# Kernel optimization log

Measured on AMD Instinct MI355X. Metric: run time of the kernel, lower is better.

## Reference

```python
import jax, jax.numpy as jnp
import numpy as np

D_MODEL = 1024
NUM_HEADS = 16
DEPTH = D_MODEL // NUM_HEADS
MAX_SEQ = 2048
B, S = 2, 2048


def setup_inputs() -> dict:
    key = jax.random.key(0)
    ks = jax.random.split(key, 12)
    scale = 1.0 / np.sqrt(D_MODEL)
    inp = {
        'q': jax.random.normal(ks[0], (B, S, D_MODEL), jnp.float32),
        'k': jax.random.normal(ks[1], (B, S, D_MODEL), jnp.float32),
        'v': jax.random.normal(ks[2], (B, S, D_MODEL), jnp.float32),
        'mask': jnp.zeros((B, 1, S, S), jnp.float32),
        'wq_w': jax.random.normal(ks[3], (D_MODEL, D_MODEL), jnp.float32) * scale,
        'wq_b': jnp.zeros((D_MODEL,), jnp.float32),
        'wk_w': jax.random.normal(ks[4], (D_MODEL, D_MODEL), jnp.float32) * scale,
        'wk_b': jnp.zeros((D_MODEL,), jnp.float32),
        'wv_w': jax.random.normal(ks[5], (D_MODEL, D_MODEL), jnp.float32) * scale,
        'wv_b': jnp.zeros((D_MODEL,), jnp.float32),
        'dense_w': jax.random.normal(ks[6], (D_MODEL, D_MODEL), jnp.float32) * scale,
        'dense_b': jnp.zeros((D_MODEL,), jnp.float32),
        'rel_bias': jax.random.normal(ks[7], (2 * MAX_SEQ - 1, NUM_HEADS), jnp.float32),
    }
    return inp


def _split_heads(x):
    # [B, S, D_MODEL] -> [B, H, S, depth]
    b, s, _ = x.shape
    return x.reshape(b, s, NUM_HEADS, DEPTH).transpose(0, 2, 1, 3)


def reference(q, k, v, mask, wq_w, wq_b, wk_w, wk_b, wv_w, wv_b, dense_w, dense_b, rel_bias):
    b, s, _ = q.shape
    # torch Linear: y = x @ W.T + b
    qh = _split_heads(q @ wq_w.T + wq_b)
    kh = _split_heads(k @ wk_w.T + wk_b)
    vh = _split_heads(v @ wv_w.T + wv_b)
    logits = jnp.einsum('bhqd,bhkd->bhqk', qh, kh) / jnp.sqrt(jnp.float32(DEPTH))
    # relative position bias gather
    pos = jnp.arange(s)
    idx = jnp.clip(pos[:, None] - pos[None, :] + MAX_SEQ - 1, 0, 2 * MAX_SEQ - 2)  # [S, S]
    pos_bias = rel_bias[idx]                      # [S, S, H]
    pos_bias = pos_bias.transpose(2, 0, 1)[None]  # [1, H, S, S]
    logits = logits + pos_bias + mask * (-1e9)
    attn = jax.nn.softmax(logits, axis=-1)        # dropout is identity in eval
    out = jnp.einsum('bhqk,bhkd->bhqd', attn, vh)
    out = out.transpose(0, 2, 1, 3).reshape(b, s, D_MODEL)
    out = out @ dense_w.T + dense_b
    return out, attn
```

## Files before the change

kernel.cpp:

```cpp
#include <hip/hip_runtime.h>

typedef _Float16 f16x8 __attribute__((ext_vector_type(8)));
typedef _Float16 f16x4 __attribute__((ext_vector_type(4)));
typedef float f32x4 __attribute__((ext_vector_type(4)));
typedef unsigned short u16x8 __attribute__((ext_vector_type(8)));
typedef unsigned int u32;

#define MFMA16H(a, b, c) __builtin_amdgcn_mfma_f32_16x16x32_f16(a, b, c, 0, 0, 0)

#if __has_builtin(__builtin_amdgcn_exp2f)
#define EXP2F(x) __builtin_amdgcn_exp2f(x)
#else
#define EXP2F(x) exp2f(x)
#endif

#define LOG2E 1.44269504088896340736f
#define SHIFT2 14.0f

__device__ __forceinline__ unsigned short f2bf(float x) {
  unsigned u = __float_as_uint(x);
  u += 0x7FFF + ((u >> 16) & 1);
  return (unsigned short)(u >> 16);
}
__device__ __forceinline__ float bf2f(unsigned short h) {
  return __uint_as_float(((unsigned)h) << 16);
}
__device__ __forceinline__ f16x8 ldh8(const _Float16* p) {
  return *reinterpret_cast<const f16x8*>(p);
}
__device__ __forceinline__ u16x8 ldu8(const unsigned short* p) {
  return *reinterpret_cast<const u16x8*>(p);
}
__device__ __forceinline__ f16x8 cvt8(float4 a, float4 b) {
  f16x8 r;
  r[0] = (_Float16)a.x; r[1] = (_Float16)a.y; r[2] = (_Float16)a.z; r[3] = (_Float16)a.w;
  r[4] = (_Float16)b.x; r[5] = (_Float16)b.y; r[6] = (_Float16)b.z; r[7] = (_Float16)b.w;
  return r;
}

__global__ __launch_bounds__(256) void prep_mask_perm(const float* __restrict__ src,
                                                      unsigned short* __restrict__ dst) {
  const int blk = blockIdx.x;
  const int kt = blk & 31, bq = blk >> 5;
  const int b = bq >> 5, qt = bq & 31;
  const int lane = threadIdx.x;
  const int w = lane >> 6, lg = (lane >> 4) & 3, lr = lane & 15;
  const int q0 = qt * 64;
  const float cs = -1e9f * LOG2E;
  unsigned short vals[16];
#pragma unroll
  for (int c = 0; c < 4; ++c)
#pragma unroll
    for (int r = 0; r < 4; ++r) {
      const int qr = q0 + w * 16 + lg * 4 + r;
      const int kc = kt * 64 + c * 16 + lr;
      vals[c * 4 + r] = f2bf(src[((size_t)b * 2048 + qr) * 2048 + kc] * cs);
    }
  uint4* out = reinterpret_cast<uint4*>(dst) + ((size_t)blk * 256 + lane) * 2;
  out[0] = *reinterpret_cast<uint4*>(&vals[0]);
  out[1] = *reinterpret_cast<uint4*>(&vals[8]);
}

__global__ __launch_bounds__(256, 3) void proj_gemm_kernel(
    const float* __restrict__ qin, const float* __restrict__ kin, const float* __restrict__ vin,
    const float* __restrict__ wq, const float* __restrict__ wk, const float* __restrict__ wv,
    const float* __restrict__ bq, const float* __restrict__ bk, const float* __restrict__ bv,
    _Float16* __restrict__ qhf, _Float16* __restrict__ khf, _Float16* __restrict__ vhT) {
  __shared__ __align__(16) _Float16 As[128 * 32];
  __shared__ __align__(16) _Float16 Bs[128 * 32];

  const int mode = blockIdx.x >> 8;
  const int t = blockIdx.x & 255;
  const float* A = mode == 0 ? qin : (mode == 1 ? kin : vin);
  const float* B = mode == 0 ? wq : (mode == 1 ? wk : wv);
  const float* bias = mode == 0 ? bq : (mode == 1 ? bk : bv);
  _Float16* outp = mode == 0 ? qhf : (mode == 1 ? khf : vhT);

  const int tid = threadIdx.x;
  const int tm = t & 31, tn = t >> 5;
  const int m0 = tm * 128, n0 = tn * 128;
  const int w = tid >> 6, l = tid & 63, lg = l >> 4, lr = l & 15;
  const int wr = w >> 1, wc = w & 1;
  const int srow = tid >> 2, scol = (tid & 3) * 8;

  f32x4 acc[4][4] = {};

  for (int kt = 0; kt < 32; ++kt) {
    const int k0 = kt * 32;
    float4 ra[2][2], rb[2][2];
#pragma unroll
    for (int it = 0; it < 2; ++it) {
      const int row = it * 64 + srow;
      const float* pa = A + (size_t)(m0 + row) * 1024 + k0 + scol;
      const float* pb = B + (size_t)(n0 + row) * 1024 + k0 + scol;
      ra[it][0] = *reinterpret_cast<const float4*>(pa);
      ra[it][1] = *reinterpret_cast<const float4*>(pa + 4);
      rb[it][0] = *reinterpret_cast<const float4*>(pb);
      rb[it][1] = *reinterpret_cast<const float4*>(pb + 4);
    }
    __syncthreads();
#pragma unroll
    for (int it = 0; it < 2; ++it) {
      const int eo = (it * 256 + tid) * 8;
      *reinterpret_cast<f16x8*>(As + eo) = cvt8(ra[it][0], ra[it][1]);
      *reinterpret_cast<f16x8*>(Bs + eo) = cvt8(rb[it][0], rb[it][1]);
    }
    __syncthreads();

    f16x8 fa[4], fb[4];
#pragma unroll
    for (int i = 0; i < 4; ++i) {
      fa[i] = ldh8(As + (wr * 64 + i * 16 + lr) * 32 + lg * 8);
      fb[i] = ldh8(Bs + (wc * 64 + i * 16 + lr) * 32 + lg * 8);
    }
#pragma unroll
    for (int i = 0; i < 4; ++i)
#pragma unroll
      for (int j = 0; j < 4; ++j)
        acc[i][j] = MFMA16H(fa[i], fb[j], acc[i][j]);
  }

#pragma unroll
  for (int i = 0; i < 4; ++i) {
    const int mrow = m0 + wr * 64 + i * 16 + lg * 4;
#pragma unroll
    for (int j = 0; j < 4; ++j) {
      const int ncol = n0 + wc * 64 + j * 16 + lr;
      const float bv = bias[ncol];
#pragma unroll
      for (int r = 0; r < 4; ++r) {
        const int m = mrow + r;
        const float v = acc[i][j][r] + bv;
        const int bb = m >> 11, s = m & 2047, hh = ncol >> 6, d = ncol & 63;
        if (mode != 2)
          outp[((size_t)(bb * 16 + hh) * 2048 + s) * 64 + d] = (_Float16)v;
        else
          outp[((size_t)(bb * 16 + hh) * 64 + d) * 2048 + s] = (_Float16)v;
      }
    }
  }
}

__global__ __launch_bounds__(256) void dense_gemm_kernel(
    const _Float16* __restrict__ A, const float* __restrict__ B,
    const float* __restrict__ bias, float* __restrict__ out_f) {
  __shared__ __align__(16) _Float16 As[128 * 32];
  __shared__ __align__(16) _Float16 Bs[128 * 32];

  const int tid = threadIdx.x;
  const int tm = blockIdx.x & 31, tn = blockIdx.x >> 5;
  const int m0 = tm * 128, n0 = tn * 128;
  const int w = tid >> 6, l = tid & 63, lg = l >> 4, lr = l & 15;
  const int wr = w >> 1, wc = w & 1;
  const int srow = tid >> 2, scol = (tid & 3) * 8;

  f32x4 acc[4][4] = {};

  for (int kt = 0; kt < 32; ++kt) {
    const int k0 = kt * 32;
    uint4 ra[2];
    float4 rb[2][2];
#pragma unroll
    for (int it = 0; it < 2; ++it) {
      const int row = it * 64 + srow;
      ra[it] = *reinterpret_cast<const uint4*>(A + (size_t)(m0 + row) * 1024 + k0 + scol);
      const float* pb = B + (size_t)(n0 + row) * 1024 + k0 + scol;
      rb[it][0] = *reinterpret_cast<const float4*>(pb);
      rb[it][1] = *reinterpret_cast<const float4*>(pb + 4);
    }
    __syncthreads();
#pragma unroll
    for (int it = 0; it < 2; ++it) {
      const int eo = (it * 256 + tid) * 8;
      *reinterpret_cast<uint4*>(As + eo) = ra[it];
      *reinterpret_cast<f16x8*>(Bs + eo) = cvt8(rb[it][0], rb[it][1]);
    }
    __syncthreads();

    f16x8 fa[4], fb[4];
#pragma unroll
    for (int i = 0; i < 4; ++i) {
      fa[i] = ldh8(As + (wr * 64 + i * 16 + lr) * 32 + lg * 8);
      fb[i] = ldh8(Bs + (wc * 64 + i * 16 + lr) * 32 + lg * 8);
    }
#pragma unroll
    for (int i = 0; i < 4; ++i)
#pragma unroll
      for (int j = 0; j < 4; ++j)
        acc[i][j] = MFMA16H(fa[i], fb[j], acc[i][j]);
  }

#pragma unroll
  for (int i = 0; i < 4; ++i) {
    const int mrow = m0 + wr * 64 + i * 16 + lg * 4;
#pragma unroll
    for (int j = 0; j < 4; ++j) {
      const int ncol = n0 + wc * 64 + j * 16 + lr;
      const float bv = bias[ncol];
#pragma unroll
      for (int r = 0; r < 4; ++r)
        out_f[(size_t)(mrow + r) * 1024 + ncol] = acc[i][j][r] + bv;
    }
  }
}

__global__ __launch_bounds__(256, 3) void attn_pv_kernel(
    const _Float16* __restrict__ qh, const _Float16* __restrict__ kh,
    const _Float16* __restrict__ vT,
    const float* __restrict__ rel_bias, const unsigned short* __restrict__ mperm,
    _Float16* __restrict__ o_h, float* __restrict__ scal) {
  __shared__ float rb2[2112];
  __shared__ __align__(16) _Float16 p_lds[64 * 76];

  const int bid = blockIdx.x;
  const int wg = ((bid & 7) << 7) | (bid >> 3);
  const int bh = wg >> 5, qt = wg & 31;
  const int b = bh >> 4, h = bh & 15;
  const int q0 = qt * 64;
  const int tid = threadIdx.x;
  const int w = tid >> 6, l = tid & 63, lg = l >> 4, lr = l & 15;

  for (int t = tid; t < 2111; t += 256)
    rb2[t] = rel_bias[(q0 + t) * 16 + h] * LOG2E - SHIFT2;

  const size_t bh_off = (size_t)bh * 2048 * 64;
  const _Float16* qhb = qh + bh_off;
  const _Float16* khb = kh + bh_off;
  const _Float16* vTb = vT + bh_off;
  const unsigned short* mpb =
      mperm + (((size_t)(b * 32 + qt) * 32) * 256 + tid) * 16;

  f16x8 qf[2];
  {
    const size_t qrow = (size_t)(q0 + w * 16 + lr) * 64;
    qf[0] = ldh8(qhb + qrow + lg * 8);
    qf[1] = ldh8(qhb + qrow + 32 + lg * 8);
  }
  __syncthreads();

  const int qbase = w * 16 + lg * 4;
  const float c1 = 0.125f * LOG2E;
  float sacc[4] = {0.f, 0.f, 0.f, 0.f};
  f32x4 acc_o[4] = {};

  for (int kt = 0; kt < 32; ++kt) {
    u16x8 m0v = ldu8(mpb + (size_t)kt * 4096);
    u16x8 m1v = ldu8(mpb + (size_t)kt * 4096 + 8);
#pragma unroll
    for (int c = 0; c < 4; ++c) {
      const int kc = kt * 64 + c * 16 + lr;
      const _Float16* kr = khb + (size_t)kc * 64 + lg * 8;
      f32x4 acc = {};
      acc = MFMA16H(qf[0], ldh8(kr), acc);
      acc = MFMA16H(qf[1], ldh8(kr + 32), acc);
#pragma unroll
      for (int r = 0; r < 4; ++r) {
        const float mbf = bf2f((c < 2) ? (unsigned short)m0v[(c & 1) * 4 + r]
                                       : (unsigned short)m1v[(c & 1) * 4 + r]);
        const float l2 = fmaf(acc[r], c1, rb2[qbase + r - kc + 2047]) + mbf;
        const float p = EXP2F(l2);
        sacc[r] += p;
        p_lds[(qbase + r) * 76 + c * 16 + lr] = (_Float16)p;
      }
    }
    f16x8 pf0 = ldh8(p_lds + (w * 16 + lr) * 76 + lg * 8);
    f16x8 pf1 = ldh8(p_lds + (w * 16 + lr) * 76 + 32 + lg * 8);
#pragma unroll
    for (int n = 0; n < 4; ++n) {
      const _Float16* vr = vTb + (size_t)(n * 16 + lr) * 2048 + kt * 64 + lg * 8;
      acc_o[n] = MFMA16H(pf0, ldh8(vr), acc_o[n]);
      acc_o[n] = MFMA16H(pf1, ldh8(vr + 32), acc_o[n]);
    }
  }

  float inv_s[4];
#pragma unroll
  for (int r = 0; r < 4; ++r) {
    float s = sacc[r];
    s += __shfl_xor(s, 1);
    s += __shfl_xor(s, 2);
    s += __shfl_xor(s, 4);
    s += __shfl_xor(s, 8);
    inv_s[r] = 1.0f / s;
    if (lr == 0) scal[(size_t)bh * 2048 + q0 + qbase + r] = inv_s[r];
  }

#pragma unroll
  for (int n = 0; n < 4; ++n)
#pragma unroll
    for (int r = 0; r < 4; ++r) {
      const int qr = q0 + qbase + r;
      const int d = n * 16 + lr;
      o_h[((size_t)(b * 2048 + qr) * 16 + h) * 64 + d] = (_Float16)(acc_o[n][r] * inv_s[r]);
    }
}

__global__ __launch_bounds__(256, 4) void attn_write_kernel(
    const _Float16* __restrict__ qh, const _Float16* __restrict__ kh,
    const float* __restrict__ rel_bias, const unsigned short* __restrict__ mperm,
    const float* __restrict__ scal, float* __restrict__ attn_out) {
  __shared__ float rb2[2112];
  __shared__ __align__(16) float p32[64 * 68];

  const int bid = blockIdx.x;
  const int wg = ((bid & 7) << 7) | (bid >> 3);
  const int bh = wg >> 5, qt = wg & 31;
  const int b = bh >> 4, h = bh & 15;
  const int q0 = qt * 64;
  const int tid = threadIdx.x;
  const int w = tid >> 6, l = tid & 63, lg = l >> 4, lr = l & 15;

  for (int t = tid; t < 2111; t += 256)
    rb2[t] = rel_bias[(q0 + t) * 16 + h] * LOG2E - SHIFT2;

  const size_t bh_off = (size_t)bh * 2048 * 64;
  const _Float16* qhb = qh + bh_off;
  const _Float16* khb = kh + bh_off;
  const unsigned short* mpb =
      mperm + (((size_t)(b * 32 + qt) * 32) * 256 + tid) * 16;
  float* attn_bh = attn_out + (size_t)bh * 2048 * 2048;

  f16x8 qf[2];
  {
    const size_t qrow = (size_t)(q0 + w * 16 + lr) * 64;
    qf[0] = ldh8(qhb + qrow + lg * 8);
    qf[1] = ldh8(qhb + qrow + 32 + lg * 8);
  }
  __syncthreads();

  const int qbase = w * 16 + lg * 4;
  const float c1 = 0.125f * LOG2E;
  float4 inv4 = *reinterpret_cast<const float4*>(scal + (size_t)bh * 2048 + q0 + qbase);
  const float invs[4] = {inv4.x, inv4.y, inv4.z, inv4.w};

  const int srow = w * 16 + (l >> 2);
  const int scb = (l & 3) * 16;

  for (int kt = 0; kt < 32; ++kt) {
    u16x8 m0v = ldu8(mpb + (size_t)kt * 4096);
    u16x8 m1v = ldu8(mpb + (size_t)kt * 4096 + 8);
#pragma unroll
    for (int c = 0; c < 4; ++c) {
      const int kc = kt * 64 + c * 16 + lr;
      const _Float16* kr = khb + (size_t)kc * 64 + lg * 8;
      f32x4 acc = {};
      acc = MFMA16H(qf[0], ldh8(kr), acc);
      acc = MFMA16H(qf[1], ldh8(kr + 32), acc);
#pragma unroll
      for (int r = 0; r < 4; ++r) {
        const float mbf = bf2f((c < 2) ? (unsigned short)m0v[(c & 1) * 4 + r]
                                       : (unsigned short)m1v[(c & 1) * 4 + r]);
        const float l2 = fmaf(acc[r], c1, rb2[qbase + r - kc + 2047]) + mbf;
        p32[(qbase + r) * 68 + c * 16 + lr] = EXP2F(l2) * invs[r];
      }
    }
    float* arow = attn_bh + (size_t)(q0 + srow) * 2048 + kt * 64 + scb;
#pragma unroll
    for (int i = 0; i < 4; ++i)
      *reinterpret_cast<float4*>(arow + i * 4) =
          *reinterpret_cast<const float4*>(&p32[srow * 68 + scb + i * 4]);
  }
}

extern "C" void kernel_launch(void* const* d_in, const int* in_sizes, int n_in,
                              void* d_out, int out_size, void* d_ws, size_t ws_size,
                              hipStream_t stream) {
  const float* q = (const float*)d_in[0];
  const float* k = (const float*)d_in[1];
  const float* v = (const float*)d_in[2];
  const float* mask = (const float*)d_in[3];
  const float* wq_w = (const float*)d_in[4];
  const float* wq_b = (const float*)d_in[5];
  const float* wk_w = (const float*)d_in[6];
  const float* wk_b = (const float*)d_in[7];
  const float* wv_w = (const float*)d_in[8];
  const float* wv_b = (const float*)d_in[9];
  const float* dw = (const float*)d_in[10];
  const float* db = (const float*)d_in[11];
  const float* rel = (const float*)d_in[12];

  char* ws = (char*)d_ws;
  _Float16* qhf  = (_Float16*)(ws + 0);
  _Float16* khf  = (_Float16*)(ws + 8388608);
  _Float16* vhT  = (_Float16*)(ws + 16777216);
  _Float16* o_h  = (_Float16*)(ws + 25165824);
  float* scal    = (float*)(ws + 33554432);
  unsigned short* mperm = (unsigned short*)(ws + 33816576);

  float* out = (float*)d_out;
  float* attn_out = out + 4194304;

  prep_mask_perm<<<2048, 256, 0, stream>>>(mask, mperm);

  proj_gemm_kernel<<<768, 256, 0, stream>>>(q, k, v, wq_w, wk_w, wv_w,
                                            wq_b, wk_b, wv_b, qhf, khf, vhT);

  attn_pv_kernel<<<1024, 256, 0, stream>>>(qhf, khf, vhT, rel, mperm, o_h, scal);
  attn_write_kernel<<<1024, 256, 0, stream>>>(qhf, khf, rel, mperm, scal, attn_out);

  dense_gemm_kernel<<<256, 256, 0, stream>>>(o_h, dw, db, out);
}
```

Before: 606.7 us.

## Store unnormalized fp16 probabilities in PV pass and rescale in a streaming fixup kernel

The second attention kernel, which recomputed QK^T, bias and exp to write the fp32 attention matrix, is removed. The PV kernel now also writes unnormalized fp16 probabilities to a workspace buffer, and a grid-stride fixup kernel scales them by the stored inverse row sums into fp32. K and mask loads in the PV loop are double-buffered in registers, and occupancy is lowered to 2 blocks per CU to make room for them. The exp shift is reduced from 14 to 5 so fp16 probabilities keep enough range. This costs an extra 128MB fp16 write plus read, and the attention output now carries fp16 rounding.

```diff
diff --git a/kernel.cpp b/kernel.cpp
--- a/kernel.cpp
+++ b/kernel.cpp
@@ -15,7 +15,7 @@
 #endif
 
 #define LOG2E 1.44269504088896340736f
-#define SHIFT2 14.0f
+#define SHIFT2 5.0f
 
 __device__ __forceinline__ unsigned short f2bf(float x) {
   unsigned u = __float_as_uint(x);
@@ -204,11 +204,12 @@
   }
 }
 
-__global__ __launch_bounds__(256, 3) void attn_pv_kernel(
+__global__ __launch_bounds__(256, 2) void attn_pv_kernel(
     const _Float16* __restrict__ qh, const _Float16* __restrict__ kh,
     const _Float16* __restrict__ vT,
     const float* __restrict__ rel_bias, const unsigned short* __restrict__ mperm,
-    _Float16* __restrict__ o_h, float* __restrict__ scal) {
+    _Float16* __restrict__ o_h, _Float16* __restrict__ p16,
+    float* __restrict__ scal) {
   __shared__ float rb2[2112];
   __shared__ __align__(16) _Float16 p_lds[64 * 76];
 
@@ -229,6 +230,7 @@
   const _Float16* vTb = vT + bh_off;
   const unsigned short* mpb =
       mperm + (((size_t)(b * 32 + qt) * 32) * 256 + tid) * 16;
+  _Float16* pbh = p16 + (size_t)bh * 2048 * 2048;
 
   f16x8 qf[2];
   {
@@ -243,20 +245,30 @@
   float sacc[4] = {0.f, 0.f, 0.f, 0.f};
   f32x4 acc_o[4] = {};
 
-  for (int kt = 0; kt < 32; ++kt) {
-    u16x8 m0v = ldu8(mpb + (size_t)kt * 4096);
-    u16x8 m1v = ldu8(mpb + (size_t)kt * 4096 + 8);
+  f16x8 kA[8], kB[8];
+  u16x8 mA[2], mB[2];
+
+  auto loadK = [&](int kt, f16x8* kd, u16x8* md) {
+    md[0] = ldu8(mpb + (size_t)kt * 4096);
+    md[1] = ldu8(mpb + (size_t)kt * 4096 + 8);
 #pragma unroll
     for (int c = 0; c < 4; ++c) {
+      const _Float16* kr = khb + (size_t)(kt * 64 + c * 16 + lr) * 64 + lg * 8;
+      kd[c * 2] = ldh8(kr);
+      kd[c * 2 + 1] = ldh8(kr + 32);
+    }
+  };
+
+  auto step = [&](int kt, const f16x8* kd, const u16x8* md) {
+#pragma unroll
+    for (int c = 0; c < 4; ++c) {
+      f32x4 acc = {};
+      acc = MFMA16H(qf[0], kd[c * 2], acc);
+      acc = MFMA16H(qf[1], kd[c * 2 + 1], acc);
       const int kc = kt * 64 + c * 16 + lr;
-      const _Float16* kr = khb + (size_t)kc * 64 + lg * 8;
-      f32x4 acc = {};
-      acc = MFMA16H(qf[0], ldh8(kr), acc);
-      acc = MFMA16H(qf[1], ldh8(kr + 32), acc);
 #pragma unroll
       for (int r = 0; r < 4; ++r) {
-        const float mbf = bf2f((c < 2) ? (unsigned short)m0v[(c & 1) * 4 + r]
-                                       : (unsigned short)m1v[(c & 1) * 4 + r]);
+        const float mbf = bf2f((unsigned short)md[c >> 1][(c & 1) * 4 + r]);
         const float l2 = fmaf(acc[r], c1, rb2[qbase + r - kc + 2047]) + mbf;
         const float p = EXP2F(l2);
         sacc[r] += p;
@@ -265,12 +277,23 @@
     }
     f16x8 pf0 = ldh8(p_lds + (w * 16 + lr) * 76 + lg * 8);
     f16x8 pf1 = ldh8(p_lds + (w * 16 + lr) * 76 + 32 + lg * 8);
+    _Float16* prow = pbh + (size_t)(q0 + w * 16 + lr) * 2048 + kt * 64 + lg * 8;
+    *reinterpret_cast<f16x8*>(prow) = pf0;
+    *reinterpret_cast<f16x8*>(prow + 32) = pf1;
 #pragma unroll
     for (int n = 0; n < 4; ++n) {
       const _Float16* vr = vTb + (size_t)(n * 16 + lr) * 2048 + kt * 64 + lg * 8;
       acc_o[n] = MFMA16H(pf0, ldh8(vr), acc_o[n]);
       acc_o[n] = MFMA16H(pf1, ldh8(vr + 32), acc_o[n]);
     }
+  };
+
+  loadK(0, kA, mA);
+  for (int kt = 0; kt < 32; kt += 2) {
+    loadK(kt + 1, kB, mB);
+    step(kt, kA, mA);
+    loadK((kt + 2) & 31, kA, mA);
+    step(kt + 1, kB, mB);
   }
 
   float inv_s[4];
@@ -295,70 +318,20 @@
     }
 }
 
-__global__ __launch_bounds__(256, 4) void attn_write_kernel(
-    const _Float16* __restrict__ qh, const _Float16* __restrict__ kh,
-    const float* __restrict__ rel_bias, const unsigned short* __restrict__ mperm,
-    const float* __restrict__ scal, float* __restrict__ attn_out) {
-  __shared__ float rb2[2112];
-  __shared__ __align__(16) float p32[64 * 68];
-
-  const int bid = blockIdx.x;
-  const int wg = ((bid & 7) << 7) | (bid >> 3);
-  const int bh = wg >> 5, qt = wg & 31;
-  const int b = bh >> 4, h = bh & 15;
-  const int q0 = qt * 64;
-  const int tid = threadIdx.x;
-  const int w = tid >> 6, l = tid & 63, lg = l >> 4, lr = l & 15;
-
-  for (int t = tid; t < 2111; t += 256)
-    rb2[t] = rel_bias[(q0 + t) * 16 + h] * LOG2E - SHIFT2;
-
-  const size_t bh_off = (size_t)bh * 2048 * 64;
-  const _Float16* qhb = qh + bh_off;
-  const _Float16* khb = kh + bh_off;
-  const unsigned short* mpb =
-      mperm + (((size_t)(b * 32 + qt) * 32) * 256 + tid) * 16;
-  float* attn_bh = attn_out + (size_t)bh * 2048 * 2048;
-
-  f16x8 qf[2];
-  {
-    const size_t qrow = (size_t)(q0 + w * 16 + lr) * 64;
-    qf[0] = ldh8(qhb + qrow + lg * 8);
-    qf[1] = ldh8(qhb + qrow + 32 + lg * 8);
-  }
-  __syncthreads();
-
-  const int qbase = w * 16 + lg * 4;
-  const float c1 = 0.125f * LOG2E;
-  float4 inv4 = *reinterpret_cast<const float4*>(scal + (size_t)bh * 2048 + q0 + qbase);
-  const float invs[4] = {inv4.x, inv4.y, inv4.z, inv4.w};
-
-  const int srow = w * 16 + (l >> 2);
-  const int scb = (l & 3) * 16;
-
-  for (int kt = 0; kt < 32; ++kt) {
-    u16x8 m0v = ldu8(mpb + (size_t)kt * 4096);
-    u16x8 m1v = ldu8(mpb + (size_t)kt * 4096 + 8);
-#pragma unroll
-    for (int c = 0; c < 4; ++c) {
-      const int kc = kt * 64 + c * 16 + lr;
-      const _Float16* kr = khb + (size_t)kc * 64 + lg * 8;
-      f32x4 acc = {};
-      acc = MFMA16H(qf[0], ldh8(kr), acc);
-      acc = MFMA16H(qf[1], ldh8(kr + 32), acc);
-#pragma unroll
-      for (int r = 0; r < 4; ++r) {
-        const float mbf = bf2f((c < 2) ? (unsigned short)m0v[(c & 1) * 4 + r]
-                                       : (unsigned short)m1v[(c & 1) * 4 + r]);
-        const float l2 = fmaf(acc[r], c1, rb2[qbase + r - kc + 2047]) + mbf;
-        p32[(qbase + r) * 68 + c * 16 + lr] = EXP2F(l2) * invs[r];
-      }
-    }
-    float* arow = attn_bh + (size_t)(q0 + srow) * 2048 + kt * 64 + scb;
-#pragma unroll
-    for (int i = 0; i < 4; ++i)
-      *reinterpret_cast<float4*>(arow + i * 4) =
-          *reinterpret_cast<const float4*>(&p32[srow * 68 + scb + i * 4]);
+__global__ __launch_bounds__(256) void fixup_kernel(const _Float16* __restrict__ p16,
+                                                    const float* __restrict__ scal,
+                                                    float* __restrict__ attn) {
+  const long long n8 = 16777216LL;
+  const long long stride = (long long)gridDim.x * 256;
+  for (long long i = (long long)blockIdx.x * 256 + threadIdx.x; i < n8; i += stride) {
+    f16x8 p = reinterpret_cast<const f16x8*>(p16)[i];
+    const float s = scal[i >> 8];
+    float4 lo = make_float4((float)p[0] * s, (float)p[1] * s,
+                            (float)p[2] * s, (float)p[3] * s);
+    float4 hi = make_float4((float)p[4] * s, (float)p[5] * s,
+                            (float)p[6] * s, (float)p[7] * s);
+    reinterpret_cast<float4*>(attn)[2 * i] = lo;
+    reinterpret_cast<float4*>(attn)[2 * i + 1] = hi;
   }
 }
 
@@ -386,6 +359,7 @@
   _Float16* o_h  = (_Float16*)(ws + 25165824);
   float* scal    = (float*)(ws + 33554432);
   unsigned short* mperm = (unsigned short*)(ws + 33816576);
+  _Float16* p16  = (_Float16*)(ws + 50593792);
 
   float* out = (float*)d_out;
   float* attn_out = out + 4194304;
@@ -395,8 +369,9 @@
   proj_gemm_kernel<<<768, 256, 0, stream>>>(q, k, v, wq_w, wk_w, wv_w,
                                             wq_b, wk_b, wv_b, qhf, khf, vhT);
 
-  attn_pv_kernel<<<1024, 256, 0, stream>>>(qhf, khf, vhT, rel, mperm, o_h, scal);
-  attn_write_kernel<<<1024, 256, 0, stream>>>(qhf, khf, rel, mperm, scal, attn_out);
+  attn_pv_kernel<<<1024, 256, 0, stream>>>(qhf, khf, vhT, rel, mperm, o_h, p16, scal);
+
+  fixup_kernel<<<4096, 256, 0, stream>>>(p16, scal, attn_out);
 
   dense_gemm_kernel<<<256, 256, 0, stream>>>(o_h, dw, db, out);
 }
```

Result: no change. 611.8 us (+0.8%).
